# Kernel optimization log

Measured on AMD Instinct MI355X. Metric: run time of the kernel, lower is better.

Reference implementation:

```python
import jax, jax.numpy as jnp
import numpy as np

IN_CAPS = 512
NUM_CAPS = 64
DIM_CAPS = 16
NUM_ROUTING = 3
BETA = 1.0  # config['Model']['temperature']
IN_DIM = 768
Q_N = 512
EPS = 1e-8


def squash(s):
    # capsule squash along last dim
    n2 = jnp.sum(s * s, axis=-1, keepdims=True)
    return (n2 / (1.0 + n2)) * s / jnp.sqrt(n2 + EPS)


def pearsonr(x, y):
    # pearson correlation along last dim, broadcasting leading dims
    xm = x - jnp.mean(x, axis=-1, keepdims=True)
    ym = y - jnp.mean(y, axis=-1, keepdims=True)
    num = jnp.sum(xm * ym, axis=-1)
    den = jnp.sqrt(jnp.sum(xm * xm, axis=-1) * jnp.sum(ym * ym, axis=-1) + EPS)
    return num / den


def setup_inputs() -> dict:
    key = jax.random.key(0)
    k1, k2, k3, k4 = jax.random.split(key, 4)
    m = jax.random.normal(k1, (IN_CAPS, IN_DIM), dtype=jnp.float32)
    q = jax.random.normal(k2, (Q_N, IN_DIM), dtype=jnp.float32)
    W_w = jax.random.normal(k3, (IN_DIM, NUM_CAPS * DIM_CAPS), dtype=jnp.float32) * 0.02
    W_b = jax.random.normal(k4, (NUM_CAPS * DIM_CAPS,), dtype=jnp.float32) * 0.02
    return {"m": m, "q": q, "W_w": W_w, "W_b": W_b}


def reference(m, q, W_w, W_b):
    nq = q.shape[0]
    hat_m = (m @ W_w + W_b).reshape(IN_CAPS, NUM_CAPS, DIM_CAPS)          # [I,C,D]
    hat_q = (q @ W_w + W_b).reshape(nq, NUM_CAPS, DIM_CAPS)               # [Q,C,D]

    m_sg = jax.lax.stop_gradient(hat_m)                                    # detached copies used in routing
    # torch expands hat_q along in_caps but updates it uniformly -> keep broadcast dim of size 1
    q_cur = jax.lax.stop_gradient(hat_q)[:, None, :, :]                    # [Q,1,C,D]

    a = jnp.zeros((nq, IN_CAPS, NUM_CAPS), dtype=hat_m.dtype)             # routing logits
    p = jnp.tanh(pearsonr(m_sg[None], q_cur))                              # [Q,I,C]

    for _ in range(NUM_ROUTING - 1):
        d = jax.nn.softmax(a / BETA, axis=2)                               # softmax over num_caps (as in torch dim=2)
        d_sum_p = d + p                                                     # [Q,I,C]
        hat_v = jnp.einsum('qic,icd->qcd', d_sum_p, m_sg)                  # sum over in_caps
        v = squash(hat_v)                                                   # [Q,C,D]
        hat_m_cos_v = jnp.einsum('icd,qcd->qic', m_sg, v)                  # [Q,I,C]
        a = a + p * hat_m_cos_v
        q_cur = (q_cur + v[:, None]) / 2.0                                  # stays [Q,1,C,D]
        p = jnp.tanh(pearsonr(m_sg[None], q_cur))

    d = jax.nn.softmax(a / BETA, axis=2)
    d_sum_p = jax.lax.stop_gradient(d + p)                                  # detached coefficients
    hat_v = jnp.einsum('qic,icd->qcd', d_sum_p, hat_m)                      # grad flows only through hat_m
    q_prime = squash(hat_v).reshape(nq, -1)                                 # [Q, C*D]
    return q_prime
```

## Files before the change

### kernel.cpp

```cpp
#include <hip/hip_runtime.h>
#include <math.h>

#define IN_CAPS 512
#define QN      512
#define IN_DIM  768
#define NCAPS   64
#define DCAPS   16
#define CD      1024

typedef _Float16 half2_t __attribute__((ext_vector_type(2)));

#if __has_builtin(__builtin_amdgcn_rcpf)
  #define RCP(x) __builtin_amdgcn_rcpf(x)
#else
  #define RCP(x) __frcp_rn(x)
#endif

__device__ __forceinline__ float tanh_pade(float x){
  const float x2 = x*x;
  const float num = fmaf(x2, x2 + 105.0f, 945.0f);
  const float den = fmaf(x2, fmaf(x2, 15.0f, 420.0f), 945.0f);
  return x * num * RCP(den);
}

template<int CTRL>
__device__ __forceinline__ float dpp_add(float v){
  int r = __builtin_amdgcn_update_dpp(0, __float_as_int(v), CTRL, 0xF, 0xF, true);
  return v + __int_as_float(r);
}

__device__ __forceinline__ float wave_sum64_all(float v){
  v = dpp_add<0xB1>(v);
  v = dpp_add<0x4E>(v);
  v = dpp_add<0x141>(v);
  v = dpp_add<0x140>(v);
  v = dpp_add<0x142>(v);
  v = dpp_add<0x143>(v);
  return __int_as_float(__builtin_amdgcn_readlane(__float_as_int(v), 63));
}

#define LD16(dst, ptr) { const float4* _p=(const float4*)(ptr); \
  float4 _a=_p[0], _b=_p[1], _c=_p[2], _d=_p[3]; \
  dst[0]=_a.x; dst[1]=_a.y; dst[2]=_a.z; dst[3]=_a.w; \
  dst[4]=_b.x; dst[5]=_b.y; dst[6]=_b.z; dst[7]=_b.w; \
  dst[8]=_c.x; dst[9]=_c.y; dst[10]=_c.z; dst[11]=_c.w; \
  dst[12]=_d.x; dst[13]=_d.y; dst[14]=_d.z; dst[15]=_d.w; }

#define ST16(ptr, src) { float4* _p=(float4*)(ptr); \
  _p[0]=make_float4(src[0],src[1],src[2],src[3]); \
  _p[1]=make_float4(src[4],src[5],src[6],src[7]); \
  _p[2]=make_float4(src[8],src[9],src[10],src[11]); \
  _p[3]=make_float4(src[12],src[13],src[14],src[15]); }

#define LDH(dst, ptrf4) { const float4* _p=(const float4*)(ptrf4); \
  float4 _a=_p[0], _b=_p[1]; \
  dst[0]=__builtin_bit_cast(half2_t,_a.x); dst[1]=__builtin_bit_cast(half2_t,_a.y); \
  dst[2]=__builtin_bit_cast(half2_t,_a.z); dst[3]=__builtin_bit_cast(half2_t,_a.w); \
  dst[4]=__builtin_bit_cast(half2_t,_b.x); dst[5]=__builtin_bit_cast(half2_t,_b.y); \
  dst[6]=__builtin_bit_cast(half2_t,_b.z); dst[7]=__builtin_bit_cast(half2_t,_b.w); }

#define CVT16(dst, h) { \
  _Pragma("unroll") for (int _j=0;_j<8;_j++){ \
    dst[2*_j]   = (float)h[_j].x; \
    dst[2*_j+1] = (float)h[_j].y; } }

#define DOT16(res, x, y) { float _e=0.f,_o=0.f; \
  _Pragma("unroll") for (int _d=0;_d<16;_d+=2){ _e = fmaf(x[_d],y[_d],_e); _o = fmaf(x[_d+1],y[_d+1],_o); } \
  res = _e+_o; }

#define ACCUM(acc, m, w) { \
  _Pragma("unroll") for (int _d=0;_d<16;_d++) acc[_d] = fmaf(w, m[_d], acc[_d]); }

#define QSTAT(qcc, s1v, qq) { \
  float qc_[16]; \
  LD16(qc_, hat + (size_t)(IN_CAPS + (qq))*CD + c*16); \
  float s_=0.f; \
  _Pragma("unroll") for (int d=0;d<16;d++) s_ += qc_[d]; \
  const float mean_ = s_*(1.0f/16.0f); \
  float n2_=0.f; \
  _Pragma("unroll") for (int d=0;d<16;d++){ qcc[d]=qc_[d]-mean_; n2_ += qcc[d]*qcc[d]; } \
  s1v = __frsqrt_rn(n2_ + 1e-12f); }

#define WDECODE() \
  const int tid = threadIdx.x; \
  const int gw  = blockIdx.x*4 + (tid >> 6); \
  const int q   = gw >> cshift; \
  const int ch  = gw & (nch-1); \
  const int c   = tid & 63;

__global__ __launch_bounds__(256) void gemm_hat(const float* __restrict__ m,
                                                const float* __restrict__ q,
                                                const float* __restrict__ Ww,
                                                float* __restrict__ hatP)
{
  __shared__ float As[16][65];
  __shared__ float Bs[16][65];
  const int tid = threadIdx.x;
  const int bm = blockIdx.y, bn = blockIdx.x, kz = blockIdx.z;
  const int tx = tid & 15, ty = tid >> 4;

  float acc[4][4];
  #pragma unroll
  for (int a=0;a<4;a++)
    #pragma unroll
    for (int b=0;b<4;b++) acc[a][b]=0.0f;

  const int r  = tid >> 2;
  const int kk = (tid & 3) << 2;
  const int row = bm*64 + r;
  const float* srcA = (row < IN_CAPS) ? (m + row*IN_DIM) : (q + (row-IN_CAPS)*IN_DIM);
  const int krow = tid >> 4;
  const int cc   = (tid & 15) << 2;

  const int kbeg = kz*(IN_DIM/4), kend = kbeg + IN_DIM/4;
  for (int k0=kbeg; k0<kend; k0+=16){
    float4 av = *(const float4*)(srcA + k0 + kk);
    As[kk+0][r]=av.x; As[kk+1][r]=av.y; As[kk+2][r]=av.z; As[kk+3][r]=av.w;
    float4 bv = *(const float4*)(Ww + (size_t)(k0+krow)*CD + bn*64 + cc);
    Bs[krow][cc+0]=bv.x; Bs[krow][cc+1]=bv.y; Bs[krow][cc+2]=bv.z; Bs[krow][cc+3]=bv.w;
    __syncthreads();
    #pragma unroll
    for (int k=0;k<16;k++){
      float a[4], b[4];
      #pragma unroll
      for (int j=0;j<4;j++) a[j] = As[k][ty*4+j];
      #pragma unroll
      for (int j=0;j<4;j++) b[j] = Bs[k][tx*4+j];
      #pragma unroll
      for (int ii=0;ii<4;ii++)
        #pragma unroll
        for (int jj=0;jj<4;jj++) acc[ii][jj] += a[ii]*b[jj];
    }
    __syncthreads();
  }
  float* dst = hatP + (size_t)kz*1048576;
  const int col0 = bn*64 + tx*4;
  #pragma unroll
  for (int ii=0;ii<4;ii++){
    const int orow = bm*64 + ty*4 + ii;
    #pragma unroll
    for (int jj=0;jj<4;jj++) dst[(size_t)orow*CD + col0 + jj] = acc[ii][jj];
  }
}

__global__ __launch_bounds__(256) void finish_kernel(const float4* __restrict__ hatP4,
                                                     const float* __restrict__ Wb,
                                                     float4* __restrict__ hat4,
                                                     _Float16* __restrict__ hatH)
{
  const int t = blockIdx.x*256 + threadIdx.x;
  const int row = t >> 8;
  const int c4  = t & 255;
  const size_t o = (size_t)row*256 + c4;
  float4 a = hatP4[o];
  float4 b = hatP4[o + 262144];
  float4 cx = hatP4[o + 524288];
  float4 d = hatP4[o + 786432];
  const float4 wb = *(const float4*)(Wb + c4*4);
  float4 r;
  r.x = a.x+b.x+cx.x+d.x+wb.x;
  r.y = a.y+b.y+cx.y+d.y+wb.y;
  r.z = a.z+b.z+cx.z+d.z+wb.z;
  r.w = a.w+b.w+cx.w+d.w+wb.w;
  hat4[o] = r;
  if (row < IN_CAPS){
    half2_t h0, h1;
    h0.x=(_Float16)r.x; h0.y=(_Float16)r.y;
    h1.x=(_Float16)r.z; h1.y=(_Float16)r.w;
    *(float2*)(hatH + (size_t)row*CD + c4*4) =
      make_float2(__builtin_bit_cast(float,h0), __builtin_bit_cast(float,h1));
  }
}

__global__ __launch_bounds__(256) void stats_kernel(const float* __restrict__ hat,
                                                    float2* __restrict__ rs,
                                                    float* __restrict__ s1g,
                                                    _Float16* __restrict__ qccH)
{
  const int t = blockIdx.x*256 + threadIdx.x;
  const int row = t >> 6, c = t & 63;
  float v[16];
  LD16(v, hat + (size_t)row*CD + c*16);
  float s=0.f;
  #pragma unroll
  for (int d=0;d<16;d++) s += v[d];
  const float mean = s*(1.0f/16.0f);
  float n2=0.f;
  #pragma unroll
  for (int d=0;d<16;d++){ float x=v[d]-mean; n2+=x*x; }
  if (row < IN_CAPS){
    rs[t] = make_float2(__frsqrt_rn(n2 + 1e-12f), s);
  } else {
    const int qr = row - IN_CAPS;
    s1g[qr*64 + c] = __frsqrt_rn(n2 + 1e-12f);
    float tbuf[8];
    #pragma unroll
    for (int j=0;j<8;j++){
      half2_t h; h.x=(_Float16)(v[2*j]-mean); h.y=(_Float16)(v[2*j+1]-mean);
      tbuf[j] = __builtin_bit_cast(float, h);
    }
    float4* dst = (float4*)(qccH + (size_t)qr*CD + c*16);
    dst[0] = make_float4(tbuf[0],tbuf[1],tbuf[2],tbuf[3]);
    dst[1] = make_float4(tbuf[4],tbuf[5],tbuf[6],tbuf[7]);
  }
}

template<bool CACHED>
__global__ __launch_bounds__(256) void pass1_kernel(const float4* __restrict__ hatH4,
                                                    const float4* __restrict__ qccH4,
                                                    const float* __restrict__ s1g,
                                                    const float2* __restrict__ rs_g,
                                                    float* __restrict__ part,
                                                    _Float16* __restrict__ n1h,
                                                    int ilen, int nch, int cshift)
{
  WDECODE();
  float qcc1[16];
  {
    half2_t qh[8];
    LDH(qh, qccH4 + (size_t)q*128 + c*2);
    CVT16(qcc1, qh);
  }
  const float s1 = s1g[q*64+c];

  float acc[16];
  #pragma unroll
  for (int d=0;d<16;d++) acc[d]=0.f;

  const int i0 = ch*ilen;
  const float4* mp = hatH4 + (size_t)i0*128 + c*2;
  const float2* rp = rs_g + i0*64 + c;
  size_t idx = ((size_t)q*512 + i0)*64 + c;
  for (int i=0;i<ilen;i+=2, mp+=256, rp+=128, idx+=128){
    half2_t ha[8], hb[8];
    LDH(ha, mp); LDH(hb, mp+128);
    float ma[16], mb[16];
    CVT16(ma, ha); CVT16(mb, hb);
    const float ra = rp[0].x, rb = rp[64].x;
    float nA, nB;
    DOT16(nA, ma, qcc1);
    DOT16(nB, mb, qcc1);
    if (CACHED){
      n1h[idx]    = (_Float16)nA;
      n1h[idx+64] = (_Float16)nB;
    }
    const float wA = 0.015625f + tanh_pade(nA*ra*s1);
    const float wB = 0.015625f + tanh_pade(nB*rb*s1);
    ACCUM(acc, ma, wA);
    ACCUM(acc, mb, wB);
  }
  ST16(part + (((size_t)(q<<cshift) + ch)*64 + c)*16, acc);
}

__global__ __launch_bounds__(256) void reduce1_kernel(const float* __restrict__ hat,
                                                      const float* __restrict__ part,
                                                      float* __restrict__ v1g,
                                                      float2* __restrict__ aux1,
                                                      int nchunk)
{
  const int tid = threadIdx.x;
  const int q = blockIdx.x*4 + (tid>>6), c = tid & 63;
  float hv[16];
  #pragma unroll
  for (int d=0;d<16;d++) hv[d]=0.f;
  const float* pp = part + ((size_t)q*nchunk*64 + c)*16;
  for (int ch=0; ch<nchunk; ch++, pp += 1024){
    float t[16]; LD16(t, pp);
    #pragma unroll
    for (int d=0;d<16;d++) hv[d]+=t[d];
  }
  float n2=0.f;
  #pragma unroll
  for (int d=0;d<16;d++) n2 += hv[d]*hv[d];
  const float sc = n2 / ((1.0f+n2)*sqrtf(n2+1e-8f));
  float v1[16]; float sv=0.f;
  #pragma unroll
  for (int d=0;d<16;d++){ v1[d]=hv[d]*sc; sv+=v1[d]; }
  ST16(v1g + ((size_t)q*64 + c)*16, v1);
  float qc[16]; LD16(qc, hat + (size_t)(IN_CAPS+q)*CD + c*16);
  float s=0.f, ss=0.f;
  #pragma unroll
  for (int d=0;d<16;d++){ const float t2 = 0.5f*(qc[d]+v1[d]); s+=t2; ss+=t2*t2; }
  const float mean = s*(1.0f/16.0f);
  aux1[q*64+c] = make_float2(__frsqrt_rn(ss - 16.0f*mean*mean + 1e-12f), sv*(1.0f/16.0f));
}

template<bool CACHED>
__global__ __launch_bounds__(256) void pass2_kernel(const float4* __restrict__ hatH4,
                                                    const float* __restrict__ hat,
                                                    const float2* __restrict__ rs_g,
                                                    const float* __restrict__ s1g,
                                                    const float* __restrict__ v1g,
                                                    const float2* __restrict__ aux1,
                                                    float* __restrict__ part,
                                                    _Float16* __restrict__ n1h,
                                                    float* __restrict__ c2f,
                                                    int ilen, int nch, int cshift)
{
  WDECODE();
  float qcc1[16]; float s1;
  if (CACHED){
    s1 = s1g[q*64+c];
  } else {
    QSTAT(qcc1, s1, q);
  }
  float v1[16];
  LD16(v1, v1g + ((size_t)q*64 + c)*16);
  const float2 a1 = aux1[q*64+c];
  const float s2 = a1.x, mv1 = a1.y;

  float acc[16];
  #pragma unroll
  for (int d=0;d<16;d++) acc[d]=0.f;

  const int i0 = ch*ilen;
  const float4* mp = hatH4 + (size_t)i0*128 + c*2;
  const float2* rp = rs_g + i0*64 + c;
  size_t idx = ((size_t)q*512 + i0)*64 + c;
  for (int i=0;i<ilen;i+=2, mp+=256, rp+=128, idx+=128){
    half2_t ha[8], hb[8];
    LDH(ha, mp); LDH(hb, mp+128);
    float ma[16], mb[16];
    CVT16(ma, ha); CVT16(mb, hb);
    const float2 ra = rp[0], rb = rp[64];
    float n1A, n1B, cvA, cvB;
    if (CACHED){
      n1A = (float)n1h[idx];
      n1B = (float)n1h[idx+64];
    } else {
      DOT16(n1A, ma, qcc1);
      DOT16(n1B, mb, qcc1);
    }
    DOT16(cvA, ma, v1);
    DOT16(cvB, mb, v1);
    const float p1A = tanh_pade(n1A*ra.x*s1);
    const float n2A = 0.5f*(n1A + cvA - mv1*ra.y);
    const float p2A = tanh_pade(n2A*ra.x*s2);
    const float p1B = tanh_pade(n1B*rb.x*s1);
    const float n2B = 0.5f*(n1B + cvB - mv1*rb.y);
    const float p2B = tanh_pade(n2B*rb.x*s2);
    const float l1A = p1A*cvA;
    const float l1B = p1B*cvB;
    if (CACHED){
      half2_t cA; cA.x = (_Float16)l1A; cA.y = (_Float16)p2A;
      half2_t cB; cB.x = (_Float16)l1B; cB.y = (_Float16)p2B;
      c2f[idx]    = __builtin_bit_cast(float, cA);
      c2f[idx+64] = __builtin_bit_cast(float, cB);
      n1h[idx]    = (_Float16)n2A;
      n1h[idx+64] = (_Float16)n2B;
    }
    const float eA = __expf(l1A);
    const float eB = __expf(l1B);
    const float SA = wave_sum64_all(eA);
    const float SB = wave_sum64_all(eB);
    const float wA = eA*RCP(SA) + p2A;
    const float wB = eB*RCP(SB) + p2B;
    ACCUM(acc, ma, wA);
    ACCUM(acc, mb, wB);
  }
  ST16(part + (((size_t)(q<<cshift) + ch)*64 + c)*16, acc);
}

__global__ __launch_bounds__(256) void reduce2_kernel(const float* __restrict__ hat,
                                                      const float* __restrict__ part,
                                                      const float* __restrict__ v1g,
                                                      float* __restrict__ v2g,
                                                      float2* __restrict__ aux2,
                                                      int nchunk)
{
  const int tid = threadIdx.x;
  const int q = blockIdx.x*4 + (tid>>6), c = tid & 63;
  float hv[16];
  #pragma unroll
  for (int d=0;d<16;d++) hv[d]=0.f;
  const float* pp = part + ((size_t)q*nchunk*64 + c)*16;
  for (int ch=0; ch<nchunk; ch++, pp += 1024){
    float t[16]; LD16(t, pp);
    #pragma unroll
    for (int d=0;d<16;d++) hv[d]+=t[d];
  }
  float n2=0.f;
  #pragma unroll
  for (int d=0;d<16;d++) n2 += hv[d]*hv[d];
  const float sc = n2 / ((1.0f+n2)*sqrtf(n2+1e-8f));
  float v2[16]; float sv=0.f;
  #pragma unroll
  for (int d=0;d<16;d++){ v2[d]=hv[d]*sc; sv+=v2[d]; }
  ST16(v2g + ((size_t)q*64 + c)*16, v2);
  float qc[16];  LD16(qc, hat + (size_t)(IN_CAPS+q)*CD + c*16);
  float v1[16];  LD16(v1, v1g + ((size_t)q*64 + c)*16);
  float s=0.f, ss=0.f;
  #pragma unroll
  for (int d=0;d<16;d++){
    const float t3 = 0.25f*qc[d] + 0.25f*v1[d] + 0.5f*v2[d];
    s+=t3; ss+=t3*t3;
  }
  const float mean = s*(1.0f/16.0f);
  aux2[q*64+c] = make_float2(__frsqrt_rn(ss - 16.0f*mean*mean + 1e-12f), sv*(1.0f/16.0f));
}

template<bool CACHED>
__global__ __launch_bounds__(256) void pass3_kernel(const float4* __restrict__ hatH4,
                                                    const float* __restrict__ hat,
                                                    const float2* __restrict__ rs_g,
                                                    const float* __restrict__ v1g,
                                                    const float* __restrict__ v2g,
                                                    const float2* __restrict__ aux1,
                                                    const float2* __restrict__ aux2,
                                                    float* __restrict__ part,
                                                    const _Float16* __restrict__ n1h,
                                                    const float* __restrict__ c2f,
                                                    int ilen, int nch, int cshift)
{
  WDECODE();
  float v2[16];
  LD16(v2, v2g + ((size_t)q*64 + c)*16);
  const float2 a2 = aux2[q*64+c];
  const float s3 = a2.x, mv2 = a2.y;

  float qcc1[16]; float s1=0.f, s2=0.f, mv1=0.f;
  float v1[16];
  if (!CACHED){
    QSTAT(qcc1, s1, q);
    LD16(v1, v1g + ((size_t)q*64 + c)*16);
    const float2 a1 = aux1[q*64+c];
    s2 = a1.x; mv1 = a1.y;
  }

  float acc[16];
  #pragma unroll
  for (int d=0;d<16;d++) acc[d]=0.f;

  const int i0 = ch*ilen;
  const float4* mp = hatH4 + (size_t)i0*128 + c*2;
  const float2* rp = rs_g + i0*64 + c;
  size_t idx = ((size_t)q*512 + i0)*64 + c;
  for (int i=0;i<ilen;i+=2, mp+=256, rp+=128, idx+=128){
    half2_t ha[8], hb[8];
    LDH(ha, mp); LDH(hb, mp+128);
    float ma[16], mb[16];
    CVT16(ma, ha); CVT16(mb, hb);
    const float2 ra = rp[0], rb = rp[64];
    float cwA, cwB;
    DOT16(cwA, ma, v2);
    DOT16(cwB, mb, v2);
    float l1A, p2A, n2A, l1B, p2B, n2B;
    if (CACHED){
      half2_t cA = __builtin_bit_cast(half2_t, c2f[idx]);
      half2_t cB = __builtin_bit_cast(half2_t, c2f[idx+64]);
      l1A = (float)cA.x; p2A = (float)cA.y;
      l1B = (float)cB.x; p2B = (float)cB.y;
      n2A = (float)n1h[idx];
      n2B = (float)n1h[idx+64];
    } else {
      float n1A, cvA, n1B, cvB;
      DOT16(n1A, ma, qcc1); DOT16(cvA, ma, v1);
      DOT16(n1B, mb, qcc1); DOT16(cvB, mb, v1);
      const float p1A = tanh_pade(n1A*ra.x*s1);
      n2A = 0.5f*(n1A + cvA - mv1*ra.y);
      p2A = tanh_pade(n2A*ra.x*s2);
      l1A = p1A*cvA;
      const float p1B = tanh_pade(n1B*rb.x*s1);
      n2B = 0.5f*(n1B + cvB - mv1*rb.y);
      p2B = tanh_pade(n2B*rb.x*s2);
      l1B = p1B*cvB;
    }
    const float n3A = 0.5f*(n2A + cwA - mv2*ra.y);
    const float p3A = tanh_pade(n3A*ra.x*s3);
    const float n3B = 0.5f*(n2B + cwB - mv2*rb.y);
    const float p3B = tanh_pade(n3B*rb.x*s3);
    const float eA = __expf(fmaf(p2A, cwA, l1A));
    const float eB = __expf(fmaf(p2B, cwB, l1B));
    const float SA = wave_sum64_all(eA);
    const float SB = wave_sum64_all(eB);
    const float wA = eA*RCP(SA) + p3A;
    const float wB = eB*RCP(SB) + p3B;
    ACCUM(acc, ma, wA);
    ACCUM(acc, mb, wB);
  }
  ST16(part + (((size_t)(q<<cshift) + ch)*64 + c)*16, acc);
}

__global__ __launch_bounds__(256) void reduce3_kernel(const float* __restrict__ part,
                                                      float* __restrict__ out,
                                                      int nchunk)
{
  const int tid = threadIdx.x;
  const int q = blockIdx.x*4 + (tid>>6), c = tid & 63;
  float hv[16];
  #pragma unroll
  for (int d=0;d<16;d++) hv[d]=0.f;
  const float* pp = part + ((size_t)q*nchunk*64 + c)*16;
  for (int ch=0; ch<nchunk; ch++, pp += 1024){
    float t[16]; LD16(t, pp);
    #pragma unroll
    for (int d=0;d<16;d++) hv[d]+=t[d];
  }
  float n2=0.f;
  #pragma unroll
  for (int d=0;d<16;d++) n2 += hv[d]*hv[d];
  const float sc = n2 / ((1.0f+n2)*sqrtf(n2+1e-8f));
  float o[16];
  #pragma unroll
  for (int d=0;d<16;d++) o[d] = hv[d]*sc;
  ST16(out + (size_t)q*CD + c*16, o);
}

extern "C" void kernel_launch(void* const* d_in, const int* in_sizes, int n_in,
                              void* d_out, int out_size, void* d_ws, size_t ws_size,
                              hipStream_t stream)
{
  const float* m  = (const float*)d_in[0];
  const float* q  = (const float*)d_in[1];
  const float* Ww = (const float*)d_in[2];
  const float* Wb = (const float*)d_in[3];
  float* out = (float*)d_out;

  char* ws = (char*)d_ws;
  float*    hat  = (float*)   (ws + 0);
  float2*   rs   = (float2*)  (ws + 4194304);
  _Float16* hatH = (_Float16*)(ws + 4456448);
  float*    s1g  = (float*)   (ws + 5505024);
  _Float16* qccH = (_Float16*)(ws + 5636096);
  float*    v1g  = (float*)   (ws + 6684672);
  float*    v2g  = (float*)   (ws + 8781824);
  float2*   aux1 = (float2*)  (ws + 10878976);
  float2*   aux2 = (float2*)  (ws + 11141120);
  const size_t base = 11403264ull;
  const size_t CACHE_BYTES = 33554432ull + 67108864ull;

  auto spanOf = [](int nc){ size_t s = (size_t)nc*2097152ull; return s < 16777216ull ? 16777216ull : s; };

  int nchunk = 16, cshift = 4;
  bool cached;
  {
    int nc = 16, cs = 4;
    while (nc > 1 && base + spanOf(nc) + CACHE_BYTES > ws_size){ nc >>= 1; cs--; }
    cached = (base + spanOf(nc) + CACHE_BYTES <= ws_size);
    if (cached){ nchunk = nc; cshift = cs; }
    else {
      while (nchunk > 1 && base + spanOf(nchunk) > ws_size){ nchunk >>= 1; cshift--; }
    }
  }
  const size_t span = spanOf(nchunk);
  float*    part = (float*)   (ws + base);
  float*    hatP = part;
  _Float16* n1h  = (_Float16*)(ws + base + span);
  float*    c2f  = (float*)   (ws + base + span + 33554432ull);

  const int ilen = 512 / nchunk;
  const int pblocks = (QN*nchunk)/4;

  dim3 g0(16,16,4);
  gemm_hat<<<g0, 256, 0, stream>>>(m, q, Ww, hatP);
  finish_kernel<<<1024, 256, 0, stream>>>((const float4*)hatP, Wb, (float4*)hat, hatH);
  stats_kernel<<<256, 256, 0, stream>>>(hat, rs, s1g, qccH);
  if (cached){
    pass1_kernel<true><<<pblocks, 256, 0, stream>>>((const float4*)hatH, (const float4*)qccH, s1g, rs, part, n1h, ilen, nchunk, cshift);
    reduce1_kernel<<<128, 256, 0, stream>>>(hat, part, v1g, aux1, nchunk);
    pass2_kernel<true><<<pblocks, 256, 0, stream>>>((const float4*)hatH, hat, rs, s1g, v1g, aux1, part, n1h, c2f, ilen, nchunk, cshift);
    reduce2_kernel<<<128, 256, 0, stream>>>(hat, part, v1g, v2g, aux2, nchunk);
    pass3_kernel<true><<<pblocks, 256, 0, stream>>>((const float4*)hatH, hat, rs, v1g, v2g, aux1, aux2, part, n1h, c2f, ilen, nchunk, cshift);
    reduce3_kernel<<<128, 256, 0, stream>>>(part, out, nchunk);
  } else {
    pass1_kernel<false><<<pblocks, 256, 0, stream>>>((const float4*)hatH, (const float4*)qccH, s1g, rs, part, n1h, ilen, nchunk, cshift);
    reduce1_kernel<<<128, 256, 0, stream>>>(hat, part, v1g, aux1, nchunk);
    pass2_kernel<false><<<pblocks, 256, 0, stream>>>((const float4*)hatH, hat, rs, s1g, v1g, aux1, part, n1h, c2f, ilen, nchunk, cshift);
    reduce2_kernel<<<128, 256, 0, stream>>>(hat, part, v1g, v2g, aux2, nchunk);
    pass3_kernel<false><<<pblocks, 256, 0, stream>>>((const float4*)hatH, hat, rs, v1g, v2g, aux1, aux2, part, n1h, c2f, ilen, nchunk, cshift);
    reduce3_kernel<<<128, 256, 0, stream>>>(part, out, nchunk);
  }
}
```

Before: 227.4 us.

## Fuse finish and stats kernels; store routing partial sums in fp16

Merges the bias-add finish kernel with the per-capsule statistics kernel, so each block stages one row in shared memory and computes the mean and norm stats without re-reading hat from global memory and without a separate launch. Separately, the per-chunk partial sums written by the three pass kernels are now stored as fp16 and widened back to float in the reduce kernels, halving that intermediate traffic. The fp16 partials lose precision in the accumulated capsule vectors. In the fused kernel only 64 of 256 threads do the stats work.

Result: faster. 196.8 us (-13.5%).

```diff
diff --git a/kernel.cpp b/kernel.cpp
--- a/kernel.cpp
+++ b/kernel.cpp
@@ -63,6 +63,12 @@
   _Pragma("unroll") for (int _j=0;_j<8;_j++){ \
     dst[2*_j]   = (float)h[_j].x; \
     dst[2*_j+1] = (float)h[_j].y; } }
+
+#define STH16(ptr, src) { float _tb[8]; \
+  _Pragma("unroll") for (int _j=0;_j<8;_j++){ half2_t _h; _h.x=(_Float16)src[2*_j]; _h.y=(_Float16)src[2*_j+1]; _tb[_j]=__builtin_bit_cast(float,_h);} \
+  float4* _p=(float4*)(ptr); \
+  _p[0]=make_float4(_tb[0],_tb[1],_tb[2],_tb[3]); \
+  _p[1]=make_float4(_tb[4],_tb[5],_tb[6],_tb[7]); }
 
 #define DOT16(res, x, y) { float _e=0.f,_o=0.f; \
   _Pragma("unroll") for (int _d=0;_d<16;_d+=2){ _e = fmaf(x[_d],y[_d],_e); _o = fmaf(x[_d+1],y[_d+1],_o); } \
@@ -143,20 +149,23 @@
   }
 }
 
-__global__ __launch_bounds__(256) void finish_kernel(const float4* __restrict__ hatP4,
-                                                     const float* __restrict__ Wb,
-                                                     float4* __restrict__ hat4,
-                                                     _Float16* __restrict__ hatH)
-{
-  const int t = blockIdx.x*256 + threadIdx.x;
-  const int row = t >> 8;
-  const int c4  = t & 255;
-  const size_t o = (size_t)row*256 + c4;
+__global__ __launch_bounds__(256) void finish_stats_kernel(const float4* __restrict__ hatP4,
+                                                           const float* __restrict__ Wb,
+                                                           float4* __restrict__ hat4,
+                                                           _Float16* __restrict__ hatH,
+                                                           float2* __restrict__ rs,
+                                                           float* __restrict__ s1g,
+                                                           _Float16* __restrict__ qccH)
+{
+  __shared__ float rowbuf[1024];
+  const int row = blockIdx.x;
+  const int t = threadIdx.x;
+  const size_t o = (size_t)row*256 + t;
   float4 a = hatP4[o];
   float4 b = hatP4[o + 262144];
   float4 cx = hatP4[o + 524288];
   float4 d = hatP4[o + 786432];
-  const float4 wb = *(const float4*)(Wb + c4*4);
+  const float4 wb = *(const float4*)(Wb + t*4);
   float4 r;
   r.x = a.x+b.x+cx.x+d.x+wb.x;
   r.y = a.y+b.y+cx.y+d.y+wb.y;
@@ -167,41 +176,38 @@
     half2_t h0, h1;
     h0.x=(_Float16)r.x; h0.y=(_Float16)r.y;
     h1.x=(_Float16)r.z; h1.y=(_Float16)r.w;
-    *(float2*)(hatH + (size_t)row*CD + c4*4) =
+    *(float2*)(hatH + (size_t)row*CD + t*4) =
       make_float2(__builtin_bit_cast(float,h0), __builtin_bit_cast(float,h1));
   }
-}
-
-__global__ __launch_bounds__(256) void stats_kernel(const float* __restrict__ hat,
-                                                    float2* __restrict__ rs,
-                                                    float* __restrict__ s1g,
-                                                    _Float16* __restrict__ qccH)
-{
-  const int t = blockIdx.x*256 + threadIdx.x;
-  const int row = t >> 6, c = t & 63;
-  float v[16];
-  LD16(v, hat + (size_t)row*CD + c*16);
-  float s=0.f;
-  #pragma unroll
-  for (int d=0;d<16;d++) s += v[d];
-  const float mean = s*(1.0f/16.0f);
-  float n2=0.f;
-  #pragma unroll
-  for (int d=0;d<16;d++){ float x=v[d]-mean; n2+=x*x; }
-  if (row < IN_CAPS){
-    rs[t] = make_float2(__frsqrt_rn(n2 + 1e-12f), s);
-  } else {
-    const int qr = row - IN_CAPS;
-    s1g[qr*64 + c] = __frsqrt_rn(n2 + 1e-12f);
-    float tbuf[8];
-    #pragma unroll
-    for (int j=0;j<8;j++){
-      half2_t h; h.x=(_Float16)(v[2*j]-mean); h.y=(_Float16)(v[2*j+1]-mean);
-      tbuf[j] = __builtin_bit_cast(float, h);
-    }
-    float4* dst = (float4*)(qccH + (size_t)qr*CD + c*16);
-    dst[0] = make_float4(tbuf[0],tbuf[1],tbuf[2],tbuf[3]);
-    dst[1] = make_float4(tbuf[4],tbuf[5],tbuf[6],tbuf[7]);
+  rowbuf[t*4+0]=r.x; rowbuf[t*4+1]=r.y; rowbuf[t*4+2]=r.z; rowbuf[t*4+3]=r.w;
+  __syncthreads();
+  if (t < 64){
+    const int c = t;
+    float v[16];
+    #pragma unroll
+    for (int dd=0;dd<16;dd++) v[dd] = rowbuf[c*16+dd];
+    float s=0.f;
+    #pragma unroll
+    for (int dd=0;dd<16;dd++) s += v[dd];
+    const float mean = s*(1.0f/16.0f);
+    float n2=0.f;
+    #pragma unroll
+    for (int dd=0;dd<16;dd++){ float x=v[dd]-mean; n2+=x*x; }
+    if (row < IN_CAPS){
+      rs[row*64+c] = make_float2(__frsqrt_rn(n2 + 1e-12f), s);
+    } else {
+      const int qr = row - IN_CAPS;
+      s1g[qr*64 + c] = __frsqrt_rn(n2 + 1e-12f);
+      float tbuf[8];
+      #pragma unroll
+      for (int j=0;j<8;j++){
+        half2_t h; h.x=(_Float16)(v[2*j]-mean); h.y=(_Float16)(v[2*j+1]-mean);
+        tbuf[j] = __builtin_bit_cast(float, h);
+      }
+      float4* dst = (float4*)(qccH + (size_t)qr*CD + c*16);
+      dst[0] = make_float4(tbuf[0],tbuf[1],tbuf[2],tbuf[3]);
+      dst[1] = make_float4(tbuf[4],tbuf[5],tbuf[6],tbuf[7]);
+    }
   }
 }
 
@@ -210,7 +216,7 @@
                                                     const float4* __restrict__ qccH4,
                                                     const float* __restrict__ s1g,
                                                     const float2* __restrict__ rs_g,
-                                                    float* __restrict__ part,
+                                                    _Float16* __restrict__ part,
                                                     _Float16* __restrict__ n1h,
                                                     int ilen, int nch, int cshift)
 {
@@ -249,11 +255,11 @@
     ACCUM(acc, ma, wA);
     ACCUM(acc, mb, wB);
   }
-  ST16(part + (((size_t)(q<<cshift) + ch)*64 + c)*16, acc);
+  STH16(part + (((size_t)(q<<cshift) + ch)*64 + c)*16, acc);
 }
 
 __global__ __launch_bounds__(256) void reduce1_kernel(const float* __restrict__ hat,
-                                                      const float* __restrict__ part,
+                                                      const _Float16* __restrict__ part,
                                                       float* __restrict__ v1g,
                                                       float2* __restrict__ aux1,
                                                       int nchunk)
@@ -263,9 +269,10 @@
   float hv[16];
   #pragma unroll
   for (int d=0;d<16;d++) hv[d]=0.f;
-  const float* pp = part + ((size_t)q*nchunk*64 + c)*16;
+  const _Float16* pp = part + ((size_t)q*nchunk*64 + c)*16;
   for (int ch=0; ch<nchunk; ch++, pp += 1024){
-    float t[16]; LD16(t, pp);
+    half2_t th[8]; LDH(th, pp);
+    float t[16]; CVT16(t, th);
     #pragma unroll
     for (int d=0;d<16;d++) hv[d]+=t[d];
   }
@@ -292,7 +299,7 @@
                                                     const float* __restrict__ s1g,
                                                     const float* __restrict__ v1g,
                                                     const float2* __restrict__ aux1,
-                                                    float* __restrict__ part,
+                                                    _Float16* __restrict__ part,
                                                     _Float16* __restrict__ n1h,
                                                     float* __restrict__ c2f,
                                                     int ilen, int nch, int cshift)
@@ -358,11 +365,11 @@
     ACCUM(acc, ma, wA);
     ACCUM(acc, mb, wB);
   }
-  ST16(part + (((size_t)(q<<cshift) + ch)*64 + c)*16, acc);
+  STH16(part + (((size_t)(q<<cshift) + ch)*64 + c)*16, acc);
 }
 
 __global__ __launch_bounds__(256) void reduce2_kernel(const float* __restrict__ hat,
-                                                      const float* __restrict__ part,
+                                                      const _Float16* __restrict__ part,
                                                       const float* __restrict__ v1g,
                                                       float* __restrict__ v2g,
                                                       float2* __restrict__ aux2,
@@ -373,9 +380,10 @@
   float hv[16];
   #pragma unroll
   for (int d=0;d<16;d++) hv[d]=0.f;
-  const float* pp = part + ((size_t)q*nchunk*64 + c)*16;
+  const _Float16* pp = part + ((size_t)q*nchunk*64 + c)*16;
   for (int ch=0; ch<nchunk; ch++, pp += 1024){
-    float t[16]; LD16(t, pp);
+    half2_t th[8]; LDH(th, pp);
+    float t[16]; CVT16(t, th);
     #pragma unroll
     for (int d=0;d<16;d++) hv[d]+=t[d];
   }
@@ -407,7 +415,7 @@
                                                     const float* __restrict__ v2g,
                                                     const float2* __restrict__ aux1,
                                                     const float2* __restrict__ aux2,
-                                                    float* __restrict__ part,
+                                                    _Float16* __restrict__ part,
                                                     const _Float16* __restrict__ n1h,
                                                     const float* __restrict__ c2f,
                                                     int ilen, int nch, int cshift)
@@ -478,10 +486,10 @@
     ACCUM(acc, ma, wA);
     ACCUM(acc, mb, wB);
   }
-  ST16(part + (((size_t)(q<<cshift) + ch)*64 + c)*16, acc);
-}
-
-__global__ __launch_bounds__(256) void reduce3_kernel(const float* __restrict__ part,
+  STH16(part + (((size_t)(q<<cshift) + ch)*64 + c)*16, acc);
+}
+
+__global__ __launch_bounds__(256) void reduce3_kernel(const _Float16* __restrict__ part,
                                                       float* __restrict__ out,
                                                       int nchunk)
 {
@@ -490,9 +498,10 @@
   float hv[16];
   #pragma unroll
   for (int d=0;d<16;d++) hv[d]=0.f;
-  const float* pp = part + ((size_t)q*nchunk*64 + c)*16;
+  const _Float16* pp = part + ((size_t)q*nchunk*64 + c)*16;
   for (int ch=0; ch<nchunk; ch++, pp += 1024){
-    float t[16]; LD16(t, pp);
+    half2_t th[8]; LDH(th, pp);
+    float t[16]; CVT16(t, th);
     #pragma unroll
     for (int d=0;d<16;d++) hv[d]+=t[d];
   }
@@ -529,7 +538,7 @@
   const size_t base = 11403264ull;
   const size_t CACHE_BYTES = 33554432ull + 67108864ull;
 
-  auto spanOf = [](int nc){ size_t s = (size_t)nc*2097152ull; return s < 16777216ull ? 16777216ull : s; };
+  auto spanOf = [](int nc){ size_t s = (size_t)nc*1048576ull; return s < 16777216ull ? 16777216ull : s; };
 
   int nchunk = 16, cshift = 4;
   bool cached;
@@ -543,8 +552,8 @@
     }
   }
   const size_t span = spanOf(nchunk);
-  float*    part = (float*)   (ws + base);
-  float*    hatP = part;
+  _Float16* part = (_Float16*)(ws + base);
+  float*    hatP = (float*)   (ws + base);
   _Float16* n1h  = (_Float16*)(ws + base + span);
   float*    c2f  = (float*)   (ws + base + span + 33554432ull);
 
@@ -553,8 +562,7 @@
 
   dim3 g0(16,16,4);
   gemm_hat<<<g0, 256, 0, stream>>>(m, q, Ww, hatP);
-  finish_kernel<<<1024, 256, 0, stream>>>((const float4*)hatP, Wb, (float4*)hat, hatH);
-  stats_kernel<<<256, 256, 0, stream>>>(hat, rs, s1g, qccH);
+  finish_stats_kernel<<<1024, 256, 0, stream>>>((const float4*)hatP, Wb, (float4*)hat, hatH, rs, s1g, qccH);
   if (cached){
     pass1_kernel<true><<<pblocks, 256, 0, stream>>>((const float4*)hatH, (const float4*)qccH, s1g, rs, part, n1h, ilen, nchunk, cshift);
     reduce1_kernel<<<128, 256, 0, stream>>>(hat, part, v1g, aux1, nchunk);
```
